# Kernel optimization log

Measured on AMD Instinct MI355X. Metric: run time of the kernel, lower is better.

The kernel has to match this reference:

```python
import jax, jax.numpy as jnp
import numpy as np

B, P, K, HE, HF = 256, 128, 512, 1024, 512
D = K + HE + 2 * HF  # 2560, MLP input dim
HID = 64


def setup_inputs() -> dict:
    key = jax.random.key(0)
    ks = jax.random.split(key, 6)
    query = jax.random.normal(ks[0], (B, 1, HE), dtype=jnp.float32)
    keys = jax.random.normal(ks[1], (B, P, K), dtype=jnp.float32)
    frameLSTM_h = jax.random.normal(ks[2], (B, 1, 2 * HF), dtype=jnp.float32)
    mask = jax.random.randint(ks[3], (B, P), 0, 2, dtype=jnp.int32)
    mask = mask.at[:, 0].set(1)  # guarantee at least one unmasked player per row
    W1 = jax.random.normal(ks[4], (D, HID), dtype=jnp.float32) / np.float32(np.sqrt(D))
    W2 = jax.random.normal(ks[5], (HID, 1), dtype=jnp.float32) / np.float32(np.sqrt(HID))
    return dict(query=query, keys=keys, frameLSTM_h=frameLSTM_h, mask=mask, W1=W1, W2=W2)


def reference(query, keys, frameLSTM_h, mask, W1, W2):
    # Faithful to: cat([keys, query.repeat, frame.repeat]) @ W1 -> ReLU -> @ W2.
    # The pre-activation is linear, so splitting W1 by row-blocks is exactly the
    # same math without materializing the repeated/concatenated (B,P,D) tensor.
    W1k = W1[:K]            # (K, 64)
    W1q = W1[K:K + HE]      # (HE, 64)
    W1f = W1[K + HE:]       # (2*HF, 64)
    h = jax.nn.relu(
        jnp.einsum('bpk,kh->bph', keys, W1k)
        + jnp.einsum('boe,eh->boh', query, W1q)        # broadcasts over P
        + jnp.einsum('bof,fh->boh', frameLSTM_h, W1f)  # broadcasts over P
    )  # (B, P, 64)
    raw_scores = jnp.einsum('bph,ho->bp', h, W2)  # (B, P)
    raw_scores = jnp.where(mask == 0, -jnp.inf, raw_scores)
    weights = jax.nn.softmax(raw_scores, axis=1)  # (B, P)
    context = jnp.einsum('bp,bpk->bk', weights, keys)[:, None, :]  # (B, 1, K)
    embeddings = jnp.concatenate([context, frameLSTM_h], axis=2)   # (B, 1, K+2*HF)
    return embeddings, weights
```

## Files before the change

### kernel.cpp

```cpp
#include <hip/hip_runtime.h>
#include <hip/hip_bf16.h>
#include <cstdint>
#include <math.h>


typedef __bf16 bf16;
typedef __attribute__((ext_vector_type(8))) __bf16 bf16x8;
typedef __attribute__((ext_vector_type(4))) float f32x4;

#define NB 256
#define NP 128
#define NK 512
#define SMEM_BYTES (65536 + 256 * 4)

__global__ __launch_bounds__(512) void prep_kernel(
    const float* __restrict__ W1, const float* __restrict__ query,
    const float* __restrict__ frame, bf16* __restrict__ w1kt,
    float* __restrict__ proj)
{
    __shared__ float s[64][65];
    __shared__ float sq[4][2048];
    __shared__ float red[8][4][64];
    const int blk = blockIdx.x;
    const int t = threadIdx.x;
    if (blk < 8) {
        const int k0 = blk * 64;
#pragma unroll
        for (int i = 0; i < 8; i++) {
            const int idx = t + 512 * i;
            const int k = idx >> 6, h = idx & 63;
            s[k][h] = W1[(size_t)(k0 + k) * 64 + h];
        }
        __syncthreads();
#pragma unroll
        for (int i = 0; i < 8; i++) {
            const int idx = t + 512 * i;
            const int h = idx >> 6, kk = idx & 63;
            w1kt[(size_t)h * 512 + k0 + kk] = (bf16)s[kk][h];
        }
    } else {
        const int b0 = (blk - 8) * 4;
#pragma unroll
        for (int i = 0; i < 4; i++) {
            const int flat = (t + 512 * i) * 4;
            const int bl = flat >> 11;
            const int d  = flat & 2047;
            const float* src = (d < 1024)
                ? (query + (size_t)(b0 + bl) * 1024 + d)
                : (frame + (size_t)(b0 + bl) * 1024 + (d - 1024));
            *(float4*)&sq[bl][d] = *(const float4*)src;
        }
        __syncthreads();

        const int w = t >> 6;
        const int h = t & 63;
        const float* w1c = W1 + (size_t)(512 + w * 256) * 64 + h;
        float wreg[4][16];
#pragma unroll
        for (int bu = 0; bu < 3; bu++)
#pragma unroll
            for (int u = 0; u < 16; u++)
                wreg[bu][u] = w1c[(size_t)(bu * 16 + u) * 64];

        float acc[4] = {0.f, 0.f, 0.f, 0.f};
#pragma unroll
        for (int rr = 0; rr < 16; rr++) {
            const int cur = rr & 3;
            if (rr < 13) {
#pragma unroll
                for (int u = 0; u < 16; u++)
                    wreg[(rr + 3) & 3][u] = w1c[(size_t)((rr + 3) * 16 + u) * 64];
            }
#pragma unroll
            for (int u4 = 0; u4 < 4; u4++) {
                float4 qv[4];
#pragma unroll
                for (int j = 0; j < 4; j++)
                    qv[j] = *(const float4*)&sq[j][w * 256 + rr * 16 + u4 * 4];
#pragma unroll
                for (int uu = 0; uu < 4; uu++) {
                    const float wv = wreg[cur][u4 * 4 + uu];
                    acc[0] += (&qv[0].x)[uu] * wv;
                    acc[1] += (&qv[1].x)[uu] * wv;
                    acc[2] += (&qv[2].x)[uu] * wv;
                    acc[3] += (&qv[3].x)[uu] * wv;
                }
            }
        }
#pragma unroll
        for (int j = 0; j < 4; j++) red[w][j][h] = acc[j];
        __syncthreads();
        if (t < 256) {
            const int j2 = t >> 6, hh = t & 63;
            float sum = 0.f;
#pragma unroll
            for (int ww = 0; ww < 8; ww++) sum += red[ww][j2][hh];
            proj[(size_t)(b0 + j2) * 64 + hh] = sum;
        }
    }
}

__global__ __launch_bounds__(512) void attn_kernel(
    const float* __restrict__ keys, const float* __restrict__ frame,
    const int* __restrict__ mask, const float* __restrict__ W2,
    const bf16* __restrict__ w1kt, const float* __restrict__ proj,
    float* __restrict__ out)
{
    extern __shared__ char smem[];
    char* sB      = smem;
    float* scores = (float*)(smem + 65536);
    float* wts    = scores + 128;

    const int b = blockIdx.x;
    const int t = threadIdx.x;
    const int w = t >> 6;
    const int lane = t & 63;
    const int m = lane & 15;
    const int q = lane >> 4;
    const int p0 = w * 16;
    const int xorv = (m & 7) << 4;

    const float* arow = keys + (size_t)b * (NP * NK) + (size_t)(p0 + m) * NK + q * 8;

    float4 Aa[8], Ab[8];
#pragma unroll
    for (int i = 0; i < 6; i++) {
        Aa[i] = *(const float4*)(arow + i * 32);
        Ab[i] = *(const float4*)(arow + i * 32 + 4);
    }

    {
        const char* wsrc = (const char*)w1kt;
#pragma unroll
        for (int i = 0; i < 8; i++) {
            const int o = i * 8192 + t * 16;
            const int row = o >> 10;
            *(bf16x8*)(sB + (o ^ ((row & 7) << 4))) = *(const bf16x8*)(wsrc + o);
        }
    }

    float pv[4], wv[4];
#pragma unroll
    for (int nt = 0; nt < 4; nt++) {
        pv[nt] = proj[b * 64 + nt * 16 + m];
        wv[nt] = W2[nt * 16 + m];
    }
    __syncthreads();

    f32x4 acc[4];
#pragma unroll
    for (int nt = 0; nt < 4; nt++) acc[nt] = (f32x4){0.f, 0.f, 0.f, 0.f};

    bf16x8 Bp[2][4];
#pragma unroll
    for (int nt = 0; nt < 4; nt++)
        Bp[0][nt] = *(const bf16x8*)(sB + nt * 16384 + m * 1024 + ((q * 16) ^ xorv));

#pragma unroll
    for (int kk = 0; kk < 16; kk++) {
        const int cur = kk & 7;
        const int bc = kk & 1;
        if (kk < 10) {
            Aa[(kk + 6) & 7] = *(const float4*)(arow + (kk + 6) * 32);
            Ab[(kk + 6) & 7] = *(const float4*)(arow + (kk + 6) * 32 + 4);
        }
        if (kk < 15) {
#pragma unroll
            for (int nt = 0; nt < 4; nt++)
                Bp[bc ^ 1][nt] = *(const bf16x8*)(sB + nt * 16384 + m * 1024
                                  + ((((kk + 1) * 64) | (q * 16)) ^ xorv));
        }
        bf16x8 Af;
        Af[0] = (bf16)Aa[cur].x; Af[1] = (bf16)Aa[cur].y;
        Af[2] = (bf16)Aa[cur].z; Af[3] = (bf16)Aa[cur].w;
        Af[4] = (bf16)Ab[cur].x; Af[5] = (bf16)Ab[cur].y;
        Af[6] = (bf16)Ab[cur].z; Af[7] = (bf16)Ab[cur].w;
#pragma unroll
        for (int nt = 0; nt < 4; nt++)
            acc[nt] = __builtin_amdgcn_mfma_f32_16x16x32_bf16(Af, Bp[bc][nt], acc[nt], 0, 0, 0);
    }

    float pr[4] = {0.f, 0.f, 0.f, 0.f};
#pragma unroll
    for (int nt = 0; nt < 4; nt++)
#pragma unroll
        for (int r = 0; r < 4; r++)
            pr[r] += fmaxf(acc[nt][r] + pv[nt], 0.f) * wv[nt];

#pragma unroll
    for (int off = 1; off < 16; off <<= 1)
#pragma unroll
        for (int r = 0; r < 4; r++)
            pr[r] += __shfl_xor(pr[r], off);

    if (m == 0) {
#pragma unroll
        for (int r = 0; r < 4; r++) scores[p0 + q * 4 + r] = pr[r];
    }
    __syncthreads();

    const float* kc = keys + (size_t)b * (NP * NK) + t;
    float kreg[2][16];
#pragma unroll
    for (int i = 0; i < 16; i++) kreg[0][i] = kc[(size_t)i * NK];

    if (t < 64) {
        const int pa = t, pb = t + 64;
        float s0 = (mask[b * 128 + pa] == 0) ? -INFINITY : scores[pa];
        float s1 = (mask[b * 128 + pb] == 0) ? -INFINITY : scores[pb];
        float mx = fmaxf(s0, s1);
#pragma unroll
        for (int off = 32; off; off >>= 1) mx = fmaxf(mx, __shfl_xor(mx, off));
        float e0 = __expf(s0 - mx), e1 = __expf(s1 - mx);
        float sum = e0 + e1;
#pragma unroll
        for (int off = 32; off; off >>= 1) sum += __shfl_xor(sum, off);
        const float inv = 1.0f / sum;
        e0 *= inv; e1 *= inv;
        wts[pa] = e0; wts[pb] = e1;
        float* wout = out + (size_t)NB * 1536;
        wout[b * 128 + pa] = e0;
        wout[b * 128 + pb] = e1;
    }
    __syncthreads();

    {
        float acc2 = 0.f;
#pragma unroll
        for (int c8 = 0; c8 < 8; c8++) {
            const int cu2 = c8 & 1;
            if (c8 < 7) {
#pragma unroll
                for (int i = 0; i < 16; i++)
                    kreg[cu2 ^ 1][i] = kc[(size_t)((c8 + 1) * 16 + i) * NK];
            }
#pragma unroll
            for (int i = 0; i < 16; i++)
                acc2 += wts[c8 * 16 + i] * kreg[cu2][i];
        }
        out[(size_t)b * 1536 + t] = acc2;
    }
    if (t < 256) {
        const float4 fv = *(const float4*)(frame + (size_t)b * 1024 + t * 4);
        *(float4*)(out + (size_t)b * 1536 + 512 + t * 4) = fv;
    }
}

extern "C" void kernel_launch(void* const* d_in, const int* in_sizes, int n_in,
                              void* d_out, int out_size, void* d_ws, size_t ws_size,
                              hipStream_t stream) {
    const float* query = (const float*)d_in[0];
    const float* keys  = (const float*)d_in[1];
    const float* frame = (const float*)d_in[2];
    const int*   mask  = (const int*)d_in[3];
    const float* W1    = (const float*)d_in[4];
    const float* W2    = (const float*)d_in[5];
    float* out = (float*)d_out;

    bf16* w1kt  = (bf16*)d_ws;
    float* proj = (float*)((char*)d_ws + (64 << 10));

    hipFuncSetAttribute((const void*)attn_kernel,
                        hipFuncAttributeMaxDynamicSharedMemorySize, SMEM_BYTES);

    prep_kernel<<<72, 512, 0, stream>>>(W1, query, frame, w1kt, proj);
    attn_kernel<<<256, 512, SMEM_BYTES, stream>>>(keys, frame, mask, W2,
                                                  w1kt, proj, out);
}
```

Before: 123.1 us.

## Fuse weight prep and query projection into the attention kernel

Removes the separate prep kernel. Each attention block now transposes and converts W1k to bf16 straight into shared memory, and computes its own query/frame projection against W1 rows 512..2559. This drops one kernel launch and the round trip through the workspace. In exchange every block redundantly reads the full 640 KB of W1 and does the transpose itself, and the keys prefetch now starts only after the projection finishes, which lengthens the critical path of each block.

```diff
diff --git a/kernel.cpp b/kernel.cpp
--- a/kernel.cpp
+++ b/kernel.cpp
@@ -11,104 +11,19 @@
 #define NB 256
 #define NP 128
 #define NK 512
-#define SMEM_BYTES (65536 + 256 * 4)
-
-__global__ __launch_bounds__(512) void prep_kernel(
-    const float* __restrict__ W1, const float* __restrict__ query,
-    const float* __restrict__ frame, bf16* __restrict__ w1kt,
-    float* __restrict__ proj)
-{
-    __shared__ float s[64][65];
-    __shared__ float sq[4][2048];
-    __shared__ float red[8][4][64];
-    const int blk = blockIdx.x;
-    const int t = threadIdx.x;
-    if (blk < 8) {
-        const int k0 = blk * 64;
-#pragma unroll
-        for (int i = 0; i < 8; i++) {
-            const int idx = t + 512 * i;
-            const int k = idx >> 6, h = idx & 63;
-            s[k][h] = W1[(size_t)(k0 + k) * 64 + h];
-        }
-        __syncthreads();
-#pragma unroll
-        for (int i = 0; i < 8; i++) {
-            const int idx = t + 512 * i;
-            const int h = idx >> 6, kk = idx & 63;
-            w1kt[(size_t)h * 512 + k0 + kk] = (bf16)s[kk][h];
-        }
-    } else {
-        const int b0 = (blk - 8) * 4;
-#pragma unroll
-        for (int i = 0; i < 4; i++) {
-            const int flat = (t + 512 * i) * 4;
-            const int bl = flat >> 11;
-            const int d  = flat & 2047;
-            const float* src = (d < 1024)
-                ? (query + (size_t)(b0 + bl) * 1024 + d)
-                : (frame + (size_t)(b0 + bl) * 1024 + (d - 1024));
-            *(float4*)&sq[bl][d] = *(const float4*)src;
-        }
-        __syncthreads();
-
-        const int w = t >> 6;
-        const int h = t & 63;
-        const float* w1c = W1 + (size_t)(512 + w * 256) * 64 + h;
-        float wreg[4][16];
-#pragma unroll
-        for (int bu = 0; bu < 3; bu++)
-#pragma unroll
-            for (int u = 0; u < 16; u++)
-                wreg[bu][u] = w1c[(size_t)(bu * 16 + u) * 64];
-
-        float acc[4] = {0.f, 0.f, 0.f, 0.f};
-#pragma unroll
-        for (int rr = 0; rr < 16; rr++) {
-            const int cur = rr & 3;
-            if (rr < 13) {
-#pragma unroll
-                for (int u = 0; u < 16; u++)
-                    wreg[(rr + 3) & 3][u] = w1c[(size_t)((rr + 3) * 16 + u) * 64];
-            }
-#pragma unroll
-            for (int u4 = 0; u4 < 4; u4++) {
-                float4 qv[4];
-#pragma unroll
-                for (int j = 0; j < 4; j++)
-                    qv[j] = *(const float4*)&sq[j][w * 256 + rr * 16 + u4 * 4];
-#pragma unroll
-                for (int uu = 0; uu < 4; uu++) {
-                    const float wv = wreg[cur][u4 * 4 + uu];
-                    acc[0] += (&qv[0].x)[uu] * wv;
-                    acc[1] += (&qv[1].x)[uu] * wv;
-                    acc[2] += (&qv[2].x)[uu] * wv;
-                    acc[3] += (&qv[3].x)[uu] * wv;
-                }
-            }
-        }
-#pragma unroll
-        for (int j = 0; j < 4; j++) red[w][j][h] = acc[j];
-        __syncthreads();
-        if (t < 256) {
-            const int j2 = t >> 6, hh = t & 63;
-            float sum = 0.f;
-#pragma unroll
-            for (int ww = 0; ww < 8; ww++) sum += red[ww][j2][hh];
-            proj[(size_t)(b0 + j2) * 64 + hh] = sum;
-        }
-    }
-}
-
-__global__ __launch_bounds__(512) void attn_kernel(
-    const float* __restrict__ keys, const float* __restrict__ frame,
-    const int* __restrict__ mask, const float* __restrict__ W2,
-    const bf16* __restrict__ w1kt, const float* __restrict__ proj,
+#define SMEM_BYTES (65536 + 8192 + 2048 + 512 + 512)
+
+__global__ __launch_bounds__(512) void fused_kernel(
+    const float* __restrict__ keys, const float* __restrict__ query,
+    const float* __restrict__ frame, const int* __restrict__ mask,
+    const float* __restrict__ W1, const float* __restrict__ W2,
     float* __restrict__ out)
 {
     extern __shared__ char smem[];
     char* sB      = smem;
-    float* scores = (float*)(smem + 65536);
+    float* sq     = (float*)(smem + 65536);
+    float* red    = sq + 2048;
+    float* scores = red + 512;
     float* wts    = scores + 128;
 
     const int b = blockIdx.x;
@@ -120,32 +35,77 @@
     const int p0 = w * 16;
     const int xorv = (m & 7) << 4;
 
+    {
+        const int d = t * 4;
+        const float* src = (d < 1024) ? (query + (size_t)b * 1024 + d)
+                                      : (frame + (size_t)b * 1024 + (d - 1024));
+        *(float4*)&sq[d] = *(const float4*)src;
+    }
+
+    {
+#pragma unroll
+        for (int i = 0; i < 8; i++) {
+            const int id = t + 512 * i;
+            const int h = id & 63;
+            const int kc = id >> 6;
+            float v[8];
+#pragma unroll
+            for (int j = 0; j < 8; j++)
+                v[j] = W1[(size_t)(kc * 8 + j) * 64 + h];
+            bf16x8 bv;
+#pragma unroll
+            for (int j = 0; j < 8; j++) bv[j] = (bf16)v[j];
+            *(bf16x8*)(sB + ((h * 1024 + kc * 16) ^ ((h & 7) << 4))) = bv;
+        }
+    }
+    __syncthreads();
+
+    {
+        const float* w1p = W1 + (size_t)(512 + w * 256) * 64 + lane;
+        float wr[4][8];
+#pragma unroll
+        for (int r0 = 0; r0 < 3; r0++)
+#pragma unroll
+            for (int j = 0; j < 8; j++)
+                wr[r0][j] = w1p[(size_t)(r0 * 8 + j) * 64];
+        float pacc = 0.f;
+#pragma unroll 4
+        for (int r = 0; r < 32; r++) {
+            const int cur = r & 3;
+            if (r < 29) {
+#pragma unroll
+                for (int j = 0; j < 8; j++)
+                    wr[(r + 3) & 3][j] = w1p[(size_t)((r + 3) * 8 + j) * 64];
+            }
+            const float4 qa = *(const float4*)&sq[w * 256 + r * 8];
+            const float4 qb = *(const float4*)&sq[w * 256 + r * 8 + 4];
+            pacc += qa.x * wr[cur][0] + qa.y * wr[cur][1]
+                  + qa.z * wr[cur][2] + qa.w * wr[cur][3]
+                  + qb.x * wr[cur][4] + qb.y * wr[cur][5]
+                  + qb.z * wr[cur][6] + qb.w * wr[cur][7];
+        }
+        red[w * 64 + lane] = pacc;
+    }
+    __syncthreads();
+
+    float pv[4], wv[4];
+#pragma unroll
+    for (int nt = 0; nt < 4; nt++) {
+        const int h = nt * 16 + m;
+        float s = 0.f;
+#pragma unroll
+        for (int ww = 0; ww < 8; ww++) s += red[ww * 64 + h];
+        pv[nt] = s;
+        wv[nt] = W2[h];
+    }
+
     const float* arow = keys + (size_t)b * (NP * NK) + (size_t)(p0 + m) * NK + q * 8;
-
     float4 Aa[8], Ab[8];
 #pragma unroll
     for (int i = 0; i < 6; i++) {
         Aa[i] = *(const float4*)(arow + i * 32);
         Ab[i] = *(const float4*)(arow + i * 32 + 4);
     }
-
-    {
-        const char* wsrc = (const char*)w1kt;
-#pragma unroll
-        for (int i = 0; i < 8; i++) {
-            const int o = i * 8192 + t * 16;
-            const int row = o >> 10;
-            *(bf16x8*)(sB + (o ^ ((row & 7) << 4))) = *(const bf16x8*)(wsrc + o);
-        }
-    }
-
-    float pv[4], wv[4];
-#pragma unroll
-    for (int nt = 0; nt < 4; nt++) {
-        pv[nt] = proj[b * 64 + nt * 16 + m];
-        wv[nt] = W2[nt * 16 + m];
-    }
-    __syncthreads();
 
     f32x4 acc[4];
 #pragma unroll
@@ -257,13 +217,9 @@
     const float* W2    = (const float*)d_in[5];
     float* out = (float*)d_out;
 
-    bf16* w1kt  = (bf16*)d_ws;
-    float* proj = (float*)((char*)d_ws + (64 << 10));
-
-    hipFuncSetAttribute((const void*)attn_kernel,
+    hipFuncSetAttribute((const void*)fused_kernel,
                         hipFuncAttributeMaxDynamicSharedMemorySize, SMEM_BYTES);
 
-    prep_kernel<<<72, 512, 0, stream>>>(W1, query, frame, w1kt, proj);
-    attn_kernel<<<256, 512, SMEM_BYTES, stream>>>(keys, frame, mask, W2,
-                                                  w1kt, proj, out);
+    fused_kernel<<<256, 512, SMEM_BYTES, stream>>>(keys, query, frame, mask,
+                                                   W1, W2, out);
 }
```

Result: faster. 119.2 us (-3.1%).
